# Optimization experiments

Measured on AMD Instinct MI355X. Metric: run time of the kernel, lower is better.

The kernel has to match this reference:

```python
import jax, jax.numpy as jnp
import numpy as np

NUM_HEADS = 12
EMB = 768
HEAD = 64
SEQ = 2048
BATCH = 2


def setup_inputs() -> dict:
    key = jax.random.key(0)
    ks = jax.random.split(key, 6)
    scale = 0.02
    x = jax.random.normal(ks[0], (BATCH, SEQ, EMB), dtype=jnp.float32)
    # per-head Q/K/V projections (bias-free, Karpathy-style HeadAttention), batched over heads
    Wq = jax.random.normal(ks[1], (NUM_HEADS, EMB, HEAD), dtype=jnp.float32) * scale
    Wk = jax.random.normal(ks[2], (NUM_HEADS, EMB, HEAD), dtype=jnp.float32) * scale
    Wv = jax.random.normal(ks[3], (NUM_HEADS, EMB, HEAD), dtype=jnp.float32) * scale
    # output projection: Linear(head_size*num_heads, emb_size)
    Wo = jax.random.normal(ks[4], (NUM_HEADS * HEAD, EMB), dtype=jnp.float32) * scale
    bo = jax.random.normal(ks[5], (EMB,), dtype=jnp.float32) * scale
    return {"x": x, "Wq": Wq, "Wk": Wk, "Wv": Wv, "Wo": Wo, "bo": bo}


def reference(x, Wq, Wk, Wv, Wo, bo):
    B, S, E = x.shape
    # batched per-head projections: [B,S,E] x [H,E,D] -> [B,H,S,D]
    q = jnp.einsum("bse,hed->bhsd", x, Wq)
    k = jnp.einsum("bse,hed->bhsd", x, Wk)
    v = jnp.einsum("bse,hed->bhsd", x, Wv)
    scale = 1.0 / jnp.sqrt(jnp.asarray(HEAD, dtype=x.dtype))
    scores = jnp.einsum("bhsd,bhtd->bhst", q, k) * scale  # [B,H,S,S]
    causal = jnp.tril(jnp.ones((S, S), dtype=bool))
    scores = jnp.where(causal, scores, jnp.asarray(-jnp.inf, dtype=scores.dtype))
    attn = jax.nn.softmax(scores, axis=-1)
    out = jnp.einsum("bhst,bhtd->bhsd", attn, v)  # [B,H,S,D]
    # concat heads along last dim: [B,S,H*D]
    out = out.transpose(0, 2, 1, 3).reshape(B, S, NUM_HEADS * HEAD)
    # output projection (dropout is identity in eval mode)
    return out @ Wo + bo
```

## Files before the change

kernel.cpp:

```cpp
#include <hip/hip_runtime.h>

#define NHEAD 12
#define EMB 768
#define HDD 64
#define SEQ 2048

typedef __attribute__((ext_vector_type(4))) float f32x4;
typedef __attribute__((ext_vector_type(8))) short short8;
typedef __attribute__((ext_vector_type(4))) short short4v;
typedef unsigned int u32;

#define GLL16(g, l)                                                            \
    __builtin_amdgcn_global_load_lds(                                          \
        (const __attribute__((address_space(1))) u32*)(g),                     \
        (__attribute__((address_space(3))) u32*)(l), 16, 0, 0)

static __device__ __forceinline__ short bf16s(float f) {
    unsigned u = __builtin_bit_cast(unsigned, f);
    u = (u + 0x7fffu + ((u >> 16) & 1u)) >> 16;
    return (short)u;
}

__global__ void k_cvt_x(const float* __restrict__ x, short* __restrict__ xb) {
    const int i = (blockIdx.x * 256 + threadIdx.x) * 8;
    const f32x4* s = (const f32x4*)(x + i);
    f32x4 a = s[0], b = s[1];
    short8 o;
    o[0] = bf16s(a[0]); o[1] = bf16s(a[1]); o[2] = bf16s(a[2]); o[3] = bf16s(a[3]);
    o[4] = bf16s(b[0]); o[5] = bf16s(b[1]); o[6] = bf16s(b[2]); o[7] = bf16s(b[3]);
    *(short8*)(xb + i) = o;
}

__global__ void k_cvt_whead(const float* __restrict__ Wq, const float* __restrict__ Wk,
                            const float* __restrict__ Wv, short* __restrict__ WqT,
                            short* __restrict__ WkT, short* __restrict__ WvT) {
    const float* W = blockIdx.z == 0 ? Wq : (blockIdx.z == 1 ? Wk : Wv);
    short* Wt = blockIdx.z == 0 ? WqT : (blockIdx.z == 1 ? WkT : WvT);
    __shared__ float tile[64][65];
    const int h = blockIdx.x, e0 = blockIdx.y * 64;
    const int t = threadIdx.x;
    const int r = t >> 2, c0 = (t & 3) * 16;
    const float* src = W + (h * EMB + e0 + r) * HDD + c0;
#pragma unroll
    for (int i = 0; i < 16; ++i) tile[r][c0 + i] = src[i];
    __syncthreads();
    short* dst = Wt + (h * HDD + r) * EMB + e0 + c0;
#pragma unroll
    for (int i = 0; i < 16; ++i) dst[i] = bf16s(tile[c0 + i][r]);
}

__global__ void k_cvt_wo(const float* __restrict__ W, short* __restrict__ Wt) {
    __shared__ float tile[64][65];
    const int k0 = blockIdx.x * 64, n0 = blockIdx.y * 64;
    const int t = threadIdx.x;
    const int r = t >> 2, c0 = (t & 3) * 16;
    const float* src = W + (k0 + r) * EMB + n0 + c0;
#pragma unroll
    for (int i = 0; i < 16; ++i) tile[r][c0 + i] = src[i];
    __syncthreads();
    short* dst = Wt + (n0 + r) * EMB + k0 + c0;
#pragma unroll
    for (int i = 0; i < 16; ++i) dst[i] = bf16s(tile[c0 + i][r]);
}

template <int MODE>
__global__ __launch_bounds__(256) void k_gemm(
        const short* __restrict__ xb, const short* __restrict__ Wt0,
        const short* __restrict__ Wt1, const short* __restrict__ Wt2,
        short* __restrict__ Qo, short* __restrict__ Ko, short* __restrict__ Vo,
        const float* __restrict__ bias, float* __restrict__ Fout) {
    __shared__ alignas(16) short As[128 * 32];
    __shared__ alignas(16) short Bs[128 * 32];
    const int t = threadIdx.x, lane = t & 63, wave = t >> 6;
    const int z = (MODE == 0) ? blockIdx.z : 0;
    const short* Ap;
    const short* Bp;
    int m0, n0;
    if (MODE == 1) {
        Ap = xb; Bp = Wt0; m0 = blockIdx.y * 128; n0 = blockIdx.x * 128;
    } else if (z == 0) {
        Ap = xb; Bp = Wt0; m0 = blockIdx.y * 128; n0 = blockIdx.x * 128;
    } else if (z == 1) {
        Ap = xb; Bp = Wt1; m0 = blockIdx.y * 128; n0 = blockIdx.x * 128;
    } else {
        Ap = Wt2; Bp = xb; m0 = blockIdx.x * 128; n0 = blockIdx.y * 128;
    }

    const int srow = lane >> 2;
    const int scolSw = ((lane & 3) ^ ((srow >> 1) & 3)) * 8;
    const short* gA = Ap + (long)(m0 + wave * 32 + srow) * EMB + scolSw;
    const short* gB = Bp + (long)(n0 + wave * 32 + srow) * EMB + scolSw;
    short* lA = As + (wave * 32) * 32;
    short* lB = Bs + (wave * 32) * 32;

    const int wm = (wave >> 1) * 64, wn = (wave & 1) * 64;
    const int fr = lane & 15, hi = lane >> 4;
    const int rdoff = (hi ^ ((fr >> 1) & 3)) * 8;

    f32x4 acc[4][4];
#pragma unroll
    for (int i = 0; i < 4; ++i)
#pragma unroll
        for (int j = 0; j < 4; ++j)
#pragma unroll
            for (int e = 0; e < 4; ++e) acc[i][j][e] = 0.f;

    for (int kk = 0; kk < EMB; kk += 32) {
        __syncthreads();
        GLL16(gA + kk, lA);
        GLL16(gA + kk + 16 * EMB, lA + 16 * 32);
        GLL16(gB + kk, lB);
        GLL16(gB + kk + 16 * EMB, lB + 16 * 32);
        __syncthreads();
        short8 af[4], bfq[4];
#pragma unroll
        for (int i = 0; i < 4; ++i)
            af[i] = *(const short8*)(As + (wm + i * 16 + fr) * 32 + rdoff);
#pragma unroll
        for (int j = 0; j < 4; ++j)
            bfq[j] = *(const short8*)(Bs + (wn + j * 16 + fr) * 32 + rdoff);
#pragma unroll
        for (int i = 0; i < 4; ++i)
#pragma unroll
            for (int j = 0; j < 4; ++j)
                acc[i][j] = __builtin_amdgcn_mfma_f32_16x16x32_bf16(af[i], bfq[j], acc[i][j], 0, 0, 0);
    }

    const int r0 = hi * 4;
#pragma unroll
    for (int i = 0; i < 4; ++i) {
#pragma unroll
        for (int j = 0; j < 4; ++j) {
            const int nbase = n0 + wn + j * 16 + fr;
            float bj = 0.f;
            if (MODE == 1) bj = bias[nbase];
#pragma unroll
            for (int r = 0; r < 4; ++r) {
                const int m = m0 + wm + i * 16 + r0 + r;
                float v = acc[i][j][r];
                if (MODE == 0) {
                    if (z == 2) {
                        const int hh = m >> 6, dd = m & 63;
                        const int bb = nbase >> 11, ss = nbase & 2047;
                        Vo[(long)((bb * NHEAD + hh) * HDD + dd) * SEQ + ss] = bf16s(v);
                    } else {
                        const int bb = m >> 11, ss = m & 2047;
                        const int hh = nbase >> 6, dd = nbase & 63;
                        short* Dst = (z == 0) ? Qo : Ko;
                        if (z == 0) v *= 0.125f;
                        Dst[(long)((bb * NHEAD + hh) * SEQ + ss) * HDD + dd] = bf16s(v);
                    }
                } else {
                    Fout[(long)m * EMB + nbase] = v + bj;
                }
            }
        }
    }
}

__global__ __launch_bounds__(512) void k_attn(
        const short* __restrict__ Q, const short* __restrict__ K,
        const short* __restrict__ VT, short* __restrict__ O) {
    __shared__ alignas(16) short Kbuf[2][64 * 72];
    __shared__ alignas(16) short Vbuf[2][64 * 72];
    __shared__ alignas(16) short Ps[8][16 * 72];
    const int bh = blockIdx.x;
    const int h = bh % NHEAD, b = bh / NHEAD;
    const int qs = (int)gridDim.y - 1 - (int)blockIdx.y;
    const int q0 = qs * 128;
    const int ntile = 2 * qs + 2;
    const int t = threadIdx.x, lane = t & 63, wave = t >> 6;
    const long base = (long)(b * NHEAD + h) * SEQ * HDD;
    const short* Qg = Q + base;
    const short* Kg = K + base;
    const short* Vg = VT + base;
    const int fr = lane & 15, hi = lane >> 4, fk = hi * 8, r0 = hi * 4;
    const int wq = q0 + wave * 16;

    short8 qf[2];
#pragma unroll
    for (int c = 0; c < 2; ++c)
        qf[c] = *(const short8*)(Qg + (long)(wq + fr) * HDD + c * 32 + fk);

    f32x4 oacc[4];
#pragma unroll
    for (int i = 0; i < 4; ++i)
#pragma unroll
        for (int e = 0; e < 4; ++e) oacc[i][e] = 0.f;
    float mrun = -3e38f, lrun = 0.f;

    const int srow = t >> 3, scol = (t & 7) * 8;
    const short* KgS = Kg + (long)srow * HDD + scol;
    const short* VgS = Vg + (long)srow * SEQ + scol;
    short* Pw = &Ps[wave][0];

    short8 kvR = *(const short8*)(KgS);
    short8 vvR = *(const short8*)(VgS);
    *(short8*)(&Kbuf[0][srow * 72 + scol]) = kvR;
    *(short8*)(&Vbuf[0][srow * 72 + scol]) = vvR;
    if (ntile > 1) {
        kvR = *(const short8*)(KgS + (long)64 * HDD);
        vvR = *(const short8*)(VgS + 64);
    }
    __syncthreads();

    for (int kt = 0; kt < ntile; ++kt) {
        const int k0 = kt * 64;
        const int cur = kt & 1;
        if (kt + 1 < ntile) {
            *(short8*)(&Kbuf[cur ^ 1][srow * 72 + scol]) = kvR;
            *(short8*)(&Vbuf[cur ^ 1][srow * 72 + scol]) = vvR;
            if (kt + 2 < ntile) {
                kvR = *(const short8*)(KgS + (long)(k0 + 128) * HDD);
                vvR = *(const short8*)(VgS + (k0 + 128));
            }
        }
        if (k0 <= wq + 15) {
            const short* Ks = &Kbuf[cur][0];
            const short* Vs = &Vbuf[cur][0];

            f32x4 st[4];
#pragma unroll
            for (int nt = 0; nt < 4; ++nt) {
                const short8 kf0 = *(const short8*)(Ks + (nt * 16 + fr) * 72 + fk);
                const short8 kf1 = *(const short8*)(Ks + (nt * 16 + fr) * 72 + 32 + fk);
#pragma unroll
                for (int e = 0; e < 4; ++e) st[nt][e] = 0.f;
                st[nt] = __builtin_amdgcn_mfma_f32_16x16x32_bf16(kf0, qf[0], st[nt], 0, 0, 0);
                st[nt] = __builtin_amdgcn_mfma_f32_16x16x32_bf16(kf1, qf[1], st[nt], 0, 0, 0);
            }

            float p[4][4];
            float pmax = -3e38f;
            if (k0 + 63 > wq) {
                const int myq = wq + fr;
#pragma unroll
                for (int nt = 0; nt < 4; ++nt)
#pragma unroll
                    for (int r = 0; r < 4; ++r) {
                        float s = st[nt][r];
                        if (k0 + nt * 16 + r0 + r > myq) s = -3e38f;
                        p[nt][r] = s;
                        pmax = fmaxf(pmax, s);
                    }
            } else {
#pragma unroll
                for (int nt = 0; nt < 4; ++nt)
#pragma unroll
                    for (int r = 0; r < 4; ++r) {
                        p[nt][r] = st[nt][r];
                        pmax = fmaxf(pmax, st[nt][r]);
                    }
            }
            pmax = fmaxf(pmax, __shfl_xor(pmax, 16, 64));
            pmax = fmaxf(pmax, __shfl_xor(pmax, 32, 64));
            const float mnew = fmaxf(mrun, pmax);
            const float corr = __expf(mrun - mnew);
            mrun = mnew;
            float rsum = 0.f;
#pragma unroll
            for (int nt = 0; nt < 4; ++nt)
#pragma unroll
                for (int r = 0; r < 4; ++r) {
                    const float e = __expf(p[nt][r] - mnew);
                    p[nt][r] = e;
                    rsum += e;
                }
            rsum += __shfl_xor(rsum, 16, 64);
            rsum += __shfl_xor(rsum, 32, 64);
            lrun = lrun * corr + rsum;
#pragma unroll
            for (int dt = 0; dt < 4; ++dt)
#pragma unroll
                for (int e = 0; e < 4; ++e) oacc[dt][e] *= corr;

#pragma unroll
            for (int nt = 0; nt < 4; ++nt) {
                short4v pk;
                pk[0] = bf16s(p[nt][0]);
                pk[1] = bf16s(p[nt][1]);
                pk[2] = bf16s(p[nt][2]);
                pk[3] = bf16s(p[nt][3]);
                *(short4v*)(Pw + fr * 72 + nt * 16 + r0) = pk;
            }

#pragma unroll
            for (int kc = 0; kc < 2; ++kc) {
                const short8 pf = *(const short8*)(Pw + fr * 72 + kc * 32 + fk);
#pragma unroll
                for (int dt = 0; dt < 4; ++dt) {
                    const short8 vf = *(const short8*)(Vs + (dt * 16 + fr) * 72 + kc * 32 + fk);
                    oacc[dt] = __builtin_amdgcn_mfma_f32_16x16x32_bf16(vf, pf, oacc[dt], 0, 0, 0);
                }
            }
        }
        __syncthreads();
    }

    short* Os = &Ps[0][0];
    const float iv = 1.0f / lrun;
#pragma unroll
    for (int dt = 0; dt < 4; ++dt)
#pragma unroll
        for (int r = 0; r < 4; ++r)
            Os[(wave * 16 + fr) * 72 + dt * 16 + r0 + r] = bf16s(oacc[dt][r] * iv);
    __syncthreads();
    {
        const int row = t >> 2, c0 = (t & 3) * 16;
        const short8 o0 = *(const short8*)(Os + row * 72 + c0);
        const short8 o1 = *(const short8*)(Os + row * 72 + c0 + 8);
        short* Og = O + (long)(b * SEQ + q0 + row) * EMB + h * HDD + c0;
        *(short8*)Og = o0;
        *(short8*)(Og + 8) = o1;
    }
}

extern "C" void kernel_launch(void* const* d_in, const int* in_sizes, int n_in,
                              void* d_out, int out_size, void* d_ws, size_t ws_size,
                              hipStream_t stream) {
    const float* x  = (const float*)d_in[0];
    const float* Wq = (const float*)d_in[1];
    const float* Wk = (const float*)d_in[2];
    const float* Wv = (const float*)d_in[3];
    const float* Wo = (const float*)d_in[4];
    const float* bo = (const float*)d_in[5];
    float* out = (float*)d_out;

    char* ws = (char*)d_ws;
    short* xb  = (short*)(ws + 0);
    short* WqT = (short*)(ws + 6291456);
    short* WkT = (short*)(ws + 7471104);
    short* WvT = (short*)(ws + 8650752);
    short* WoT = (short*)(ws + 9830400);
    short* Qb  = (short*)(ws + 11010048);
    short* Kb  = (short*)(ws + 17301504);
    short* VTb = (short*)(ws + 23592960);
    short* Ob  = (short*)(ws + 29884416);

    k_cvt_x<<<dim3(1536), dim3(256), 0, stream>>>(x, xb);
    k_cvt_whead<<<dim3(12, 12, 3), dim3(256), 0, stream>>>(Wq, Wk, Wv, WqT, WkT, WvT);
    k_cvt_wo<<<dim3(12, 12), dim3(256), 0, stream>>>(Wo, WoT);
    k_gemm<0><<<dim3(6, 32, 3), dim3(256), 0, stream>>>(
        xb, WqT, WkT, WvT, Qb, Kb, VTb, (const float*)nullptr, (float*)nullptr);
    k_attn<<<dim3(24, 16), dim3(512), 0, stream>>>(Qb, Kb, VTb, Ob);
    k_gemm<1><<<dim3(6, 32, 1), dim3(256), 0, stream>>>(
        Ob, WoT, (const short*)nullptr, (const short*)nullptr,
        (short*)nullptr, (short*)nullptr, (short*)nullptr, bo, out);
}
```

Measured before the change: 105.7 us.

## Merge conversion kernels and halve attention block query tile to 64 rows

The three fp32-to-bf16 conversion and transpose kernels become one launch that dispatches on block index, removing two kernel launches. The attention kernel now uses 256 threads and 64 query rows per block instead of 512 threads and 128 rows, doubling the grid to 768 blocks. Each thread loads two 16-byte K/V chunks per tile instead of one. The aim is more blocks for load balance and occupancy across CUs on the causal workload, at the cost of each K/V tile being reloaded by twice as many blocks.

After: 100.1 us. -5.3%, faster.

```diff
diff --git a/kernel.cpp b/kernel.cpp
--- a/kernel.cpp
+++ b/kernel.cpp
@@ -21,46 +21,47 @@
     return (short)u;
 }
 
-__global__ void k_cvt_x(const float* __restrict__ x, short* __restrict__ xb) {
-    const int i = (blockIdx.x * 256 + threadIdx.x) * 8;
-    const f32x4* s = (const f32x4*)(x + i);
-    f32x4 a = s[0], b = s[1];
-    short8 o;
-    o[0] = bf16s(a[0]); o[1] = bf16s(a[1]); o[2] = bf16s(a[2]); o[3] = bf16s(a[3]);
-    o[4] = bf16s(b[0]); o[5] = bf16s(b[1]); o[6] = bf16s(b[2]); o[7] = bf16s(b[3]);
-    *(short8*)(xb + i) = o;
-}
-
-__global__ void k_cvt_whead(const float* __restrict__ Wq, const float* __restrict__ Wk,
-                            const float* __restrict__ Wv, short* __restrict__ WqT,
-                            short* __restrict__ WkT, short* __restrict__ WvT) {
-    const float* W = blockIdx.z == 0 ? Wq : (blockIdx.z == 1 ? Wk : Wv);
-    short* Wt = blockIdx.z == 0 ? WqT : (blockIdx.z == 1 ? WkT : WvT);
-    __shared__ float tile[64][65];
-    const int h = blockIdx.x, e0 = blockIdx.y * 64;
-    const int t = threadIdx.x;
-    const int r = t >> 2, c0 = (t & 3) * 16;
-    const float* src = W + (h * EMB + e0 + r) * HDD + c0;
-#pragma unroll
-    for (int i = 0; i < 16; ++i) tile[r][c0 + i] = src[i];
-    __syncthreads();
-    short* dst = Wt + (h * HDD + r) * EMB + e0 + c0;
-#pragma unroll
-    for (int i = 0; i < 16; ++i) dst[i] = bf16s(tile[c0 + i][r]);
-}
-
-__global__ void k_cvt_wo(const float* __restrict__ W, short* __restrict__ Wt) {
-    __shared__ float tile[64][65];
-    const int k0 = blockIdx.x * 64, n0 = blockIdx.y * 64;
-    const int t = threadIdx.x;
-    const int r = t >> 2, c0 = (t & 3) * 16;
-    const float* src = W + (k0 + r) * EMB + n0 + c0;
-#pragma unroll
-    for (int i = 0; i < 16; ++i) tile[r][c0 + i] = src[i];
-    __syncthreads();
-    short* dst = Wt + (n0 + r) * EMB + k0 + c0;
-#pragma unroll
-    for (int i = 0; i < 16; ++i) dst[i] = bf16s(tile[c0 + i][r]);
+__global__ void k_cvt_all(const float* __restrict__ x, const float* __restrict__ Wq,
+                          const float* __restrict__ Wk, const float* __restrict__ Wv,
+                          const float* __restrict__ Wo, short* __restrict__ xb,
+                          short* __restrict__ WqT, short* __restrict__ WkT,
+                          short* __restrict__ WvT, short* __restrict__ WoT) {
+    const int bid = blockIdx.x, t = threadIdx.x;
+    if (bid < 1536) {
+        const int i = (bid * 256 + t) * 8;
+        const f32x4* s = (const f32x4*)(x + i);
+        f32x4 a = s[0], b = s[1];
+        short8 o;
+        o[0] = bf16s(a[0]); o[1] = bf16s(a[1]); o[2] = bf16s(a[2]); o[3] = bf16s(a[3]);
+        o[4] = bf16s(b[0]); o[5] = bf16s(b[1]); o[6] = bf16s(b[2]); o[7] = bf16s(b[3]);
+        *(short8*)(xb + i) = o;
+    } else if (bid < 1968) {
+        const int idx = bid - 1536;
+        const int h = idx % 12, e0 = ((idx / 12) % 12) * 64, z = idx / 144;
+        const float* W = z == 0 ? Wq : (z == 1 ? Wk : Wv);
+        short* Wt = z == 0 ? WqT : (z == 1 ? WkT : WvT);
+        __shared__ float tile[64][65];
+        const int r = t >> 2, c0 = (t & 3) * 16;
+        const float* src = W + (h * EMB + e0 + r) * HDD + c0;
+#pragma unroll
+        for (int i = 0; i < 16; ++i) tile[r][c0 + i] = src[i];
+        __syncthreads();
+        short* dst = Wt + (h * HDD + r) * EMB + e0 + c0;
+#pragma unroll
+        for (int i = 0; i < 16; ++i) dst[i] = bf16s(tile[c0 + i][r]);
+    } else {
+        const int idx = bid - 1968;
+        const int k0 = (idx % 12) * 64, n0 = (idx / 12) * 64;
+        __shared__ float tile[64][65];
+        const int r = t >> 2, c0 = (t & 3) * 16;
+        const float* src = Wo + (k0 + r) * EMB + n0 + c0;
+#pragma unroll
+        for (int i = 0; i < 16; ++i) tile[r][c0 + i] = src[i];
+        __syncthreads();
+        short* dst = WoT + (n0 + r) * EMB + k0 + c0;
+#pragma unroll
+        for (int i = 0; i < 16; ++i) dst[i] = bf16s(tile[c0 + i][r]);
+    }
 }
 
 template <int MODE>
@@ -158,17 +159,17 @@
     }
 }
 
-__global__ __launch_bounds__(512) void k_attn(
+__global__ __launch_bounds__(256) void k_attn(
         const short* __restrict__ Q, const short* __restrict__ K,
         const short* __restrict__ VT, short* __restrict__ O) {
     __shared__ alignas(16) short Kbuf[2][64 * 72];
     __shared__ alignas(16) short Vbuf[2][64 * 72];
-    __shared__ alignas(16) short Ps[8][16 * 72];
+    __shared__ alignas(16) short Ps[4][16 * 72];
     const int bh = blockIdx.x;
     const int h = bh % NHEAD, b = bh / NHEAD;
     const int qs = (int)gridDim.y - 1 - (int)blockIdx.y;
-    const int q0 = qs * 128;
-    const int ntile = 2 * qs + 2;
+    const int q0 = qs * 64;
+    const int ntile = qs + 1;
     const int t = threadIdx.x, lane = t & 63, wave = t >> 6;
     const long base = (long)(b * NHEAD + h) * SEQ * HDD;
     const short* Qg = Q + base;
@@ -189,18 +190,24 @@
         for (int e = 0; e < 4; ++e) oacc[i][e] = 0.f;
     float mrun = -3e38f, lrun = 0.f;
 
-    const int srow = t >> 3, scol = (t & 7) * 8;
-    const short* KgS = Kg + (long)srow * HDD + scol;
-    const short* VgS = Vg + (long)srow * SEQ + scol;
+    const int srow = t >> 2, sc = (t & 3) * 16;
+    const short* KgS = Kg + (long)srow * HDD + sc;
+    const short* VgS = Vg + (long)srow * SEQ + sc;
     short* Pw = &Ps[wave][0];
 
-    short8 kvR = *(const short8*)(KgS);
-    short8 vvR = *(const short8*)(VgS);
-    *(short8*)(&Kbuf[0][srow * 72 + scol]) = kvR;
-    *(short8*)(&Vbuf[0][srow * 72 + scol]) = vvR;
+    short8 kv0 = *(const short8*)(KgS);
+    short8 kv1 = *(const short8*)(KgS + 8);
+    short8 vv0 = *(const short8*)(VgS);
+    short8 vv1 = *(const short8*)(VgS + 8);
+    *(short8*)(&Kbuf[0][srow * 72 + sc]) = kv0;
+    *(short8*)(&Kbuf[0][srow * 72 + sc + 8]) = kv1;
+    *(short8*)(&Vbuf[0][srow * 72 + sc]) = vv0;
+    *(short8*)(&Vbuf[0][srow * 72 + sc + 8]) = vv1;
     if (ntile > 1) {
-        kvR = *(const short8*)(KgS + (long)64 * HDD);
-        vvR = *(const short8*)(VgS + 64);
+        kv0 = *(const short8*)(KgS + (long)64 * HDD);
+        kv1 = *(const short8*)(KgS + (long)64 * HDD + 8);
+        vv0 = *(const short8*)(VgS + 64);
+        vv1 = *(const short8*)(VgS + 64 + 8);
     }
     __syncthreads();
 
@@ -208,11 +215,15 @@
         const int k0 = kt * 64;
         const int cur = kt & 1;
         if (kt + 1 < ntile) {
-            *(short8*)(&Kbuf[cur ^ 1][srow * 72 + scol]) = kvR;
-            *(short8*)(&Vbuf[cur ^ 1][srow * 72 + scol]) = vvR;
+            *(short8*)(&Kbuf[cur ^ 1][srow * 72 + sc]) = kv0;
+            *(short8*)(&Kbuf[cur ^ 1][srow * 72 + sc + 8]) = kv1;
+            *(short8*)(&Vbuf[cur ^ 1][srow * 72 + sc]) = vv0;
+            *(short8*)(&Vbuf[cur ^ 1][srow * 72 + sc + 8]) = vv1;
             if (kt + 2 < ntile) {
-                kvR = *(const short8*)(KgS + (long)(k0 + 128) * HDD);
-                vvR = *(const short8*)(VgS + (k0 + 128));
+                kv0 = *(const short8*)(KgS + (long)(k0 + 128) * HDD);
+                kv1 = *(const short8*)(KgS + (long)(k0 + 128) * HDD + 8);
+                vv0 = *(const short8*)(VgS + (k0 + 128));
+                vv1 = *(const short8*)(VgS + (k0 + 128) + 8);
             }
         }
         if (k0 <= wq + 15) {
@@ -337,12 +348,11 @@
     short* VTb = (short*)(ws + 23592960);
     short* Ob  = (short*)(ws + 29884416);
 
-    k_cvt_x<<<dim3(1536), dim3(256), 0, stream>>>(x, xb);
-    k_cvt_whead<<<dim3(12, 12, 3), dim3(256), 0, stream>>>(Wq, Wk, Wv, WqT, WkT, WvT);
-    k_cvt_wo<<<dim3(12, 12), dim3(256), 0, stream>>>(Wo, WoT);
+    k_cvt_all<<<dim3(2112), dim3(256), 0, stream>>>(
+        x, Wq, Wk, Wv, Wo, xb, WqT, WkT, WvT, WoT);
     k_gemm<0><<<dim3(6, 32, 3), dim3(256), 0, stream>>>(
         xb, WqT, WkT, WvT, Qb, Kb, VTb, (const float*)nullptr, (float*)nullptr);
-    k_attn<<<dim3(24, 16), dim3(512), 0, stream>>>(Qb, Kb, VTb, Ob);
+    k_attn<<<dim3(24, 32), dim3(256), 0, stream>>>(Qb, Kb, VTb, Ob);
     k_gemm<1><<<dim3(6, 32, 1), dim3(256), 0, stream>>>(
         Ob, WoT, (const short*)nullptr, (const short*)nullptr,
         (short*)nullptr, (short*)nullptr, (short*)nullptr, bo, out);
```
